# Kernel tuning notes

Hardware: AMD Instinct MI355X
Metric: run time of the kernel (lower is better)

The kernel has to match this reference:

```python
import jax, jax.numpy as jnp
import numpy as np

N = 50000      # nodes
E = 800000     # edges
DIM = 64       # dim_h (= input_dim)
H = 4          # heads
D = DIM // H   # per-head dim = 16
EDGE_DIM = 16
L = 5          # conv layers
G = 64         # graphs in batch
FINAL = 1
SCALE = 1.0 / np.sqrt(D)


def setup_inputs() -> dict:
    key = jax.random.key(0)
    ks = jax.random.split(key, 12)
    x = jax.random.normal(ks[0], (N, DIM), jnp.float32)
    edge_index = jax.random.randint(ks[1], (2, E), 0, N, dtype=jnp.int32).astype(jnp.int64)
    edge_attr = jax.random.normal(ks[2], (E, EDGE_DIM), jnp.float32)
    batch = jnp.sort(jax.random.randint(ks[3], (N,), 0, G, dtype=jnp.int32).astype(jnp.int64))
    s = 1.0 / np.sqrt(DIM)
    se = 1.0 / np.sqrt(EDGE_DIM)
    Wq = jax.random.normal(ks[4], (L, DIM, DIM), jnp.float32) * s
    Wk = jax.random.normal(ks[5], (L, DIM, DIM), jnp.float32) * s
    Wv = jax.random.normal(ks[6], (L, DIM, DIM), jnp.float32) * s
    We = jax.random.normal(ks[7], (L, EDGE_DIM, DIM), jnp.float32) * se
    Wskip = jax.random.normal(ks[8], (L, DIM, DIM), jnp.float32) * s
    W1 = jax.random.normal(ks[9], (L * DIM, L * DIM), jnp.float32) * (1.0 / np.sqrt(L * DIM))
    b1 = jnp.zeros((L * DIM,), jnp.float32)
    W2 = jax.random.normal(ks[10], (L * DIM, FINAL), jnp.float32) * (1.0 / np.sqrt(L * DIM))
    b2 = jnp.zeros((FINAL,), jnp.float32)
    return dict(x=x, edge_index=edge_index, edge_attr=edge_attr, batch=batch,
                Wq=Wq, Wk=Wk, Wv=Wv, We=We, Wskip=Wskip, W1=W1, b1=b1, W2=W2, b2=b2)


def _conv(x, Wq, Wk, Wv, We, Wsk, src, dst, edge_attr):
    # Edge-featured multi-head attention conv (EINv1 / TransformerConv-style).
    n = x.shape[0]
    q = (x @ Wq).reshape(n, H, D)[dst]                      # [E,H,D] query from dst node
    e = (edge_attr @ We).reshape(-1, H, D)                  # [E,H,D] edge projection
    k = (x @ Wk).reshape(n, H, D)[src] + e                  # [E,H,D]
    v = (x @ Wv).reshape(n, H, D)[src] + e                  # [E,H,D]
    logits = (q * k).sum(-1) * SCALE                        # [E,H]
    m = jax.ops.segment_max(logits, dst, num_segments=n)    # per-dst-node max
    a = jnp.exp(logits - m[dst])
    s = jax.ops.segment_sum(a, dst, num_segments=n)
    alpha = a / (s[dst] + 1e-16)                            # segment softmax over incoming edges
    agg = jax.ops.segment_sum(alpha[..., None] * v, dst, num_segments=n)  # [N,H,D]
    return agg.reshape(n, H * D) + x @ Wsk                  # root/skip connection


def reference(x, edge_index, edge_attr, batch, Wq, Wk, Wv, We, Wskip, W1, b1, W2, b2):
    src, dst = edge_index[0], edge_index[1]
    counts = jax.ops.segment_sum(jnp.ones((x.shape[0],), x.dtype), batch, num_segments=G)
    denom = jnp.maximum(counts, 1.0)[:, None]
    h = x
    pooled = []
    for l in range(L):  # fixed small layer count
        h = jax.nn.relu(_conv(h, Wq[l], Wk[l], Wv[l], We[l], Wskip[l], src, dst, edge_attr))
        pooled.append(jax.ops.segment_sum(h, batch, num_segments=G) / denom)  # global_mean_pool
    hcat = jnp.concatenate(pooled, axis=1)                  # [G, 5*DIM]
    hid = jax.nn.relu(hcat @ W1 + b1)
    out = hid @ W2 + b2                                     # dropout is identity in eval
    return out.reshape(-1)                                  # flatten -> [G*FINAL]
```

## Files before the change

kernel.cpp:

```cpp
#include <hip/hip_runtime.h>
#include <math.h>

#define NN 50000
#define NE 800000
#define GG 64
#define SCAN_BLK 512
#define SCAN_NB ((NN + SCAN_BLK - 1) / SCAN_BLK)
#define CSR_CAP (NE + 4 * NN)
#define NBLK ((NN + 63) / 64)

typedef unsigned int uint;
typedef unsigned short ushort;
typedef __attribute__((ext_vector_type(8))) short short8v;
typedef __attribute__((ext_vector_type(4))) float f32x4;

__device__ __forceinline__ uint bf16r(float x) {
    uint u = __float_as_uint(x);
    return (u + 0x7fffu + ((u >> 16) & 1u)) >> 16;
}

__device__ __forceinline__ float red16(float x) {
    float t;
    t = __int_as_float(__builtin_amdgcn_update_dpp(0, __float_as_int(x), 0xB1, 0xF, 0xF, 1));
    x += t;
    t = __int_as_float(__builtin_amdgcn_update_dpp(0, __float_as_int(x), 0x4E, 0xF, 0xF, 1));
    x += t;
    t = __int_as_float(__builtin_amdgcn_update_dpp(0, __float_as_int(x), 0x124, 0xF, 0xF, 1));
    x += t;
    t = __int_as_float(__builtin_amdgcn_update_dpp(0, __float_as_int(x), 0x128, 0xF, 0xF, 1));
    x += t;
    return x;
}


__global__ void k_bounds(const int* __restrict__ batch, int* __restrict__ bstart,
                         float* __restrict__ inv) {
    __shared__ int sb[65];
    int t = threadIdx.x;
    if (t <= 64) {
        int lo = 0, hi = NN;
        while (lo < hi) { int mid = (lo + hi) >> 1; if (batch[mid] < t) lo = mid + 1; else hi = mid; }
        sb[t] = lo;
        bstart[t] = lo;
    }
    __syncthreads();
    if (t < 64) inv[t] = 1.0f / fmaxf((float)(sb[t + 1] - sb[t]), 1.0f);
}


__global__ __launch_bounds__(256) void k_degrank(const int* __restrict__ dstv,
                                                 int* __restrict__ deg,
                                                 int* __restrict__ rank) {
    int e = blockIdx.x * 256 + threadIdx.x;
    if (e < NE) rank[e] = atomicAdd(&deg[dstv[e]], 1);
}

__global__ __launch_bounds__(SCAN_BLK) void k_scan1(const int* __restrict__ deg,
                                                    int* __restrict__ locoff,
                                                    int* __restrict__ bsum) {
    __shared__ int sh[SCAN_BLK];
    int tid = threadIdx.x;
    int n = blockIdx.x * SCAN_BLK + tid;
    int v = (n < NN) ? ((deg[n] + 3) & ~3) : 0;
    sh[tid] = v;
    __syncthreads();
    for (int off = 1; off < SCAN_BLK; off <<= 1) {
        int t = (tid >= off) ? sh[tid - off] : 0;
        __syncthreads();
        sh[tid] += t;
        __syncthreads();
    }
    if (n < NN) locoff[n] = sh[tid] - v;
    if (tid == SCAN_BLK - 1) bsum[blockIdx.x] = sh[tid];
}

__global__ void k_scan2(int* __restrict__ bsum) {
    __shared__ int sh[128];
    int t = threadIdx.x;
    int v = (t < SCAN_NB) ? bsum[t] : 0;
    sh[t] = v;
    __syncthreads();
    for (int off = 1; off < 128; off <<= 1) {
        int u = (t >= off) ? sh[t - off] : 0;
        __syncthreads();
        sh[t] += u;
        __syncthreads();
    }
    if (t < SCAN_NB) bsum[t] = sh[t] - v;
}

__global__ __launch_bounds__(256) void k_scan3(const int* __restrict__ locoff,
                                               const int* __restrict__ bsum,
                                               int* __restrict__ off) {
    int n = blockIdx.x * 256 + threadIdx.x;
    if (n < NN) off[n] = locoff[n] + bsum[n >> 9];
}

__global__ __launch_bounds__(256) void k_fill(const int* __restrict__ srcv,
                                              const int* __restrict__ dstv,
                                              const float* __restrict__ eattr,
                                              const int* __restrict__ off,
                                              const int* __restrict__ rank,
                                              int* __restrict__ srcp,
                                              ushort* __restrict__ aperm) {
    int e = blockIdx.x * 256 + threadIdx.x;
    if (e >= NE) return;
    int d = dstv[e];
    int p = off[d] + rank[e];
    srcp[p] = srcv[e] << 8;
    const float4* ea = reinterpret_cast<const float4*>(eattr + (size_t)e * 16);
    float4 a = ea[0], b = ea[1], c = ea[2], d4 = ea[3];
    uint4 u0, u1;
    u0.x = bf16r(a.x) | (bf16r(a.y) << 16);
    u0.y = bf16r(a.z) | (bf16r(a.w) << 16);
    u0.z = bf16r(b.x) | (bf16r(b.y) << 16);
    u0.w = bf16r(b.z) | (bf16r(b.w) << 16);
    u1.x = bf16r(c.x) | (bf16r(c.y) << 16);
    u1.y = bf16r(c.z) | (bf16r(c.w) << 16);
    u1.z = bf16r(d4.x) | (bf16r(d4.y) << 16);
    u1.w = bf16r(d4.z) | (bf16r(d4.w) << 16);
    uint4* ap = reinterpret_cast<uint4*>(aperm + (size_t)p * 16);
    ap[0] = u0;
    ap[1] = u1;
}

__global__ __launch_bounds__(256) void k_M(const float* __restrict__ Wq,
                                           const float* __restrict__ We,
                                           float* __restrict__ M) {
    int t = blockIdx.x * 256 + threadIdx.x;
    if (t >= 5 * 64 * 64) return;
    int l = t >> 12, i = (t >> 6) & 63, c = t & 63;
    int hh = c >> 4, j = c & 15;
    const float* wq = Wq + l * 4096 + i * 64 + hh * 16;
    const float* we = We + l * 1024 + j * 64 + hh * 16;
    float acc = 0.f;
#pragma unroll
    for (int dd = 0; dd < 16; ++dd) acc += wq[dd] * we[dd];
    M[t] = acc;
}


__global__ __launch_bounds__(256) void k_wfrag(const float* __restrict__ Wq,
                                               const float* __restrict__ Wk,
                                               const float* __restrict__ Wv,
                                               const float* __restrict__ Wsk,
                                               const float* __restrict__ Mw,
                                               ushort* __restrict__ Wf) {
    int t = blockIdx.x * 256 + threadIdx.x;
    if (t >= 5 * 20 * 2 * 64) return;
    int l = t / (20 * 2 * 64);
    int rem = t % (20 * 2 * 64);
    int nt = rem >> 7, s = (rem >> 6) & 1, lane = rem & 63;
    int c = nt * 16 + (lane & 15);
    int k0 = s * 32 + 8 * (lane >> 4);
    int msel = c >> 6, cc = c & 63;
    const float* W = (msel == 0) ? Wq + l * 4096 :
                     (msel == 1) ? Wk + l * 4096 :
                     (msel == 2) ? Wv + l * 4096 :
                     (msel == 3) ? Wsk + l * 4096 : Mw + l * 4096;
    ushort o[8];
#pragma unroll
    for (int j = 0; j < 8; ++j) o[j] = (ushort)bf16r(W[(k0 + j) * 64 + cc]);
    uint4* dst = reinterpret_cast<uint4*>(Wf + (size_t)t * 8);
    uint4 u;
    u.x = (uint)o[0] | ((uint)o[1] << 16);
    u.y = (uint)o[2] | ((uint)o[3] << 16);
    u.z = (uint)o[4] | ((uint)o[5] << 16);
    u.w = (uint)o[6] | ((uint)o[7] << 16);
    dst[0] = u;
}


template<bool L0>
__global__ __launch_bounds__(256) void k_projm(const float* __restrict__ x,
                                               const ushort* __restrict__ Hin,
                                               const ushort* __restrict__ Wfl,
                                               uint* __restrict__ QQp,
                                               uint* __restrict__ KVp,
                                               float* __restrict__ Sb) {
    int tid = threadIdx.x, lane = tid & 63, wv = tid >> 6;
    int n0 = blockIdx.x * 64;
    int arow = lane & 15, agrp = lane >> 4;

    short8v A[4][2];
#pragma unroll
    for (int mt = 0; mt < 4; ++mt) {
        int node = n0 + mt * 16 + arow;
        if (node >= NN) node = NN - 1;
#pragma unroll
        for (int s = 0; s < 2; ++s) {
            int k0 = s * 32 + agrp * 8;
            if (L0) {
                const float* hp = x + (size_t)node * 64 + k0;
                float4 u = *reinterpret_cast<const float4*>(hp);
                float4 v = *reinterpret_cast<const float4*>(hp + 4);
                short8v a;
                a[0] = (short)bf16r(u.x); a[1] = (short)bf16r(u.y);
                a[2] = (short)bf16r(u.z); a[3] = (short)bf16r(u.w);
                a[4] = (short)bf16r(v.x); a[5] = (short)bf16r(v.y);
                a[6] = (short)bf16r(v.z); a[7] = (short)bf16r(v.w);
                A[mt][s] = a;
            } else {
                A[mt][s] = *reinterpret_cast<const short8v*>(Hin + (size_t)node * 64 + k0);
            }
        }
    }

    int ch = wv * 16 + arow;
    int rb = agrp * 4;
    f32x4 qh[4], kh[4];
    const f32x4 z = {0.f, 0.f, 0.f, 0.f};

#pragma unroll
    for (int ni = 0; ni < 5; ++ni) {
        int ntl = wv + 4 * ni;
        f32x4 acc[4] = {z, z, z, z};
#pragma unroll
        for (int s = 0; s < 2; ++s) {
            short8v B = *reinterpret_cast<const short8v*>(
                Wfl + (((size_t)ntl * 2 + s) * 64 + lane) * 8);
#pragma unroll
            for (int mt = 0; mt < 4; ++mt)
                acc[mt] = __builtin_amdgcn_mfma_f32_16x16x32_bf16(A[mt][s], B, acc[mt], 0, 0, 0);
        }
        if (ni == 0) {
#pragma unroll
            for (int mt = 0; mt < 4; ++mt) qh[mt] = acc[mt];
        } else if (ni == 1) {
#pragma unroll
            for (int mt = 0; mt < 4; ++mt) kh[mt] = acc[mt];
        } else if (ni == 2) {
#pragma unroll
            for (int mt = 0; mt < 4; ++mt)
#pragma unroll
                for (int r = 0; r < 4; ++r) {
                    int node = n0 + mt * 16 + rb + r;
                    if (node < NN)
                        KVp[(size_t)node * 64 + ch] = (bf16r(kh[mt][r]) << 16) | bf16r(acc[mt][r]);
                }
        } else if (ni == 3) {
#pragma unroll
            for (int mt = 0; mt < 4; ++mt)
#pragma unroll
                for (int r = 0; r < 4; ++r) {
                    int node = n0 + mt * 16 + rb + r;
                    if (node < NN) Sb[(size_t)node * 64 + ch] = acc[mt][r];
                }
        } else {
#pragma unroll
            for (int mt = 0; mt < 4; ++mt)
#pragma unroll
                for (int r = 0; r < 4; ++r) {
                    int node = n0 + mt * 16 + rb + r;
                    if (node < NN)
                        QQp[(size_t)node * 64 + ch] = (bf16r(qh[mt][r]) << 16) | bf16r(acc[mt][r]);
                }
        }
    }
}


__global__ __launch_bounds__(256) void k_attn(const uint* __restrict__ QQp,
                                              const uint* __restrict__ KVp,
                                              const float* __restrict__ Sb,
                                              const float* __restrict__ Wel,
                                              const ushort* __restrict__ aperm,
                                              const int* __restrict__ srcp,
                                              const int* __restrict__ offp,
                                              const int* __restrict__ cnt,
                                              ushort* __restrict__ Hout) {
    __shared__ float we[16 * 64];
    int tid = threadIdx.x;
    for (int i = tid; i < 1024; i += 256) we[i] = Wel[i];
    __syncthreads();

    int lane = tid & 63;
    int n = blockIdx.x * 4 + (tid >> 6);
    if (n >= NN) return;

    int dd = lane & 15;
    int hg = lane >> 4;

    const float C2 = 0.36067376022224085f;
    uint qq = QQp[n * 64 + lane];
    float q  = __uint_as_float(qq & 0xffff0000u) * C2;
    float qw = __uint_as_float(qq << 16) * C2;
    int dg   = cnt[n];
    int pos0 = offp[n];
    int nbt  = (dg + 3) >> 2;

    const char* kvb = (const char*)KVp + lane * 4;
    const ushort* apb = aperm + (size_t)pos0 * 16 + dd;

    float m = -1e30f, s = 0.f, av = 0.f, aa = 0.f;

    auto ldidx = [&](int b, int4& sn) {
        sn = (b < nbt) ? *reinterpret_cast<const int4*>(srcp + pos0 + b * 4)
                       : make_int4(0, 0, 0, 0);
    };
    auto issue = [&](int b, const int4& sn, uint (&kv)[4], uint (&au)[4]) {
        kv[0] = *reinterpret_cast<const uint*>(kvb + sn.x);
        kv[1] = *reinterpret_cast<const uint*>(kvb + sn.y);
        kv[2] = *reinterpret_cast<const uint*>(kvb + sn.z);
        kv[3] = *reinterpret_cast<const uint*>(kvb + sn.w);
        const ushort* ap = apb + (size_t)b * 64;
        au[0] = ap[0];
        au[1] = ap[16];
        au[2] = ap[32];
        au[3] = ap[48];
    };
    auto compute = [&](int b, const uint (&kv)[4], const uint (&au)[4]) {
        int rem = dg - b * 4;
        float l[4], vf[4], af[4];
#pragma unroll
        for (int j = 0; j < 4; ++j) {
            uint w = kv[j];
            float kf = __uint_as_float(w & 0xffff0000u);
            vf[j] = __uint_as_float(w << 16);
            af[j] = __uint_as_float(au[j] << 16);
            float p = fmaf(q, kf, qw * af[j]);
            p = red16(p);
            l[j] = (j < rem) ? p : -1e30f;
        }
        float bm = fmaxf(fmaxf(l[0], l[1]), fmaxf(l[2], l[3]));
        float mn = fmaxf(m, bm);
        float wold = __builtin_amdgcn_exp2f(m - mn);
        float a0 = __builtin_amdgcn_exp2f(l[0] - mn);
        float a1 = __builtin_amdgcn_exp2f(l[1] - mn);
        float a2 = __builtin_amdgcn_exp2f(l[2] - mn);
        float a3 = __builtin_amdgcn_exp2f(l[3] - mn);
        s  = fmaf(s,  wold, (a0 + a1) + (a2 + a3));
        av = fmaf(av, wold, fmaf(a0, vf[0], fmaf(a1, vf[1], fmaf(a2, vf[2], a3 * vf[3]))));
        aa = fmaf(aa, wold, fmaf(a0, af[0], fmaf(a1, af[1], fmaf(a2, af[2], a3 * af[3]))));
        m = mn;
    };

    int4 sn0, sn1;
    uint kv0[4], kv1[4], at0[4], at1[4];

    ldidx(0, sn0);
    issue(0, sn0, kv0, at0);
    ldidx(1, sn1);

    int b = 0;
    while (b + 1 < nbt) {
        issue(b + 1, sn1, kv1, at1);
        ldidx(b + 2, sn0);
        compute(b, kv0, at0);
        if (b + 2 < nbt) {
            issue(b + 2, sn0, kv0, at0);
            ldidx(b + 3, sn1);
        }
        compute(b + 1, kv1, at1);
        b += 2;
    }
    if (b < nbt) compute(b, kv0, at0);

    float rden = 1.0f / (s + 1e-16f);
    float eagg = 0.f;
#pragma unroll
    for (int j = 0; j < 16; ++j) {
        float aj = __shfl(aa, hg * 16 + j, 64);
        eagg = fmaf(aj, we[j * 64 + lane], eagg);
    }
    float agg = (av + eagg) * rden;
    float hn = fmaxf(agg + Sb[n * 64 + lane], 0.f);
    Hout[(size_t)n * 64 + lane] = (ushort)bf16r(hn);
}


__global__ __launch_bounds__(512) void k_pool5(const ushort* __restrict__ Hb,
                                               const int* __restrict__ bstart,
                                               const float* __restrict__ inv,
                                               float* __restrict__ hcat) {
    __shared__ float red[512];
    int l = blockIdx.x >> 6, g = blockIdx.x & 63;
    int lo = bstart[g], hi = bstart[g + 1];
    const ushort* H = Hb + (size_t)l * NN * 64;
    int ch = threadIdx.x & 63, ro = threadIdx.x >> 6;
    float acc = 0.f;
    for (int r = lo + ro; r < hi; r += 8)
        acc += __uint_as_float((uint)H[(size_t)r * 64 + ch] << 16);
    red[threadIdx.x] = acc;
    __syncthreads();
    if (ro < 4) red[threadIdx.x] += red[threadIdx.x + 256];
    __syncthreads();
    if (ro < 2) red[threadIdx.x] += red[threadIdx.x + 128];
    __syncthreads();
    if (ro == 0)
        hcat[g * 320 + l * 64 + ch] = (red[ch] + red[64 + ch]) * inv[g];
}


__global__ __launch_bounds__(256) void k_mlp(const float* __restrict__ hcat,
                                             const float* __restrict__ W1,
                                             const float* __restrict__ b1,
                                             const float* __restrict__ W2,
                                             const float* __restrict__ b2,
                                             float* __restrict__ out) {
    __shared__ float hc[320];
    __shared__ float red[256];
    int g = blockIdx.x, tid = threadIdx.x;
    for (int i = tid; i < 320; i += 256) hc[i] = hcat[g * 320 + i];
    __syncthreads();
    float part = 0.f;
    for (int j = tid; j < 320; j += 256) {
        float t = b1[j];
        for (int k = 0; k < 320; ++k) t = fmaf(hc[k], W1[k * 320 + j], t);
        part = fmaf(fmaxf(t, 0.f), W2[j], part);
    }
    red[tid] = part;
    __syncthreads();
    for (int off = 128; off > 0; off >>= 1) {
        if (tid < off) red[tid] += red[tid + off];
        __syncthreads();
    }
    if (tid == 0) out[g] = red[0] + b2[0];
}


extern "C" void kernel_launch(void* const* d_in, const int* in_sizes, int n_in,
                              void* d_out, int out_size, void* d_ws, size_t ws_size,
                              hipStream_t stream) {
    const float* x     = (const float*)d_in[0];
    const int*   ei    = (const int*)d_in[1];
    const float* eattr = (const float*)d_in[2];
    const int*   batch = (const int*)d_in[3];
    const float* Wq    = (const float*)d_in[4];
    const float* Wk    = (const float*)d_in[5];
    const float* Wv    = (const float*)d_in[6];
    const float* We    = (const float*)d_in[7];
    const float* Wsk   = (const float*)d_in[8];
    const float* W1    = (const float*)d_in[9];
    const float* b1    = (const float*)d_in[10];
    const float* W2    = (const float*)d_in[11];
    const float* b2    = (const float*)d_in[12];
    float* out = (float*)d_out;

    const int* srcv = ei;
    const int* dstv = ei + NE;

    float* ws = (float*)d_ws;
    size_t o = 0;
    uint*   QQp = (uint*)(ws + o); o += (size_t)NN * 64;
    uint*   KVp = (uint*)(ws + o); o += (size_t)NN * 64;
    float*  Sb  = ws + o;          o += (size_t)NN * 64;
    ushort* Hb  = (ushort*)(ws + o); o += (size_t)5 * NN * 64 / 2;
    float*  Mw  = ws + o;          o += 5 * 4096;
    ushort* Wf  = (ushort*)(ws + o); o += 5 * 20 * 2 * 64 * 8 / 2;
    float*  inv = ws + o;          o += GG;
    float*  hcat = ws + o;         o += GG * 320;
    int*    bstart = (int*)(ws + o); o += 68;
    int*    deg  = (int*)(ws + o); o += NN;
    int*    srcp = (int*)(ws + o); o += CSR_CAP;
    size_t  zwords = (size_t)NN + CSR_CAP;
    int*    rank   = (int*)(ws + o); o += NE;
    int*    off    = (int*)(ws + o); o += NN;
    int*    locoff = (int*)(ws + o); o += NN;
    int*    bsum   = (int*)(ws + o); o += 128;
    ushort* aperm  = (ushort*)(ws + o); o += (size_t)CSR_CAP * 8;

    hipMemsetAsync(deg, 0, zwords * 4, stream);

    k_bounds<<<1, 128, 0, stream>>>(batch, bstart, inv);
    k_degrank<<<(NE + 255) / 256, 256, 0, stream>>>(dstv, deg, rank);
    k_scan1<<<SCAN_NB, SCAN_BLK, 0, stream>>>(deg, locoff, bsum);
    k_scan2<<<1, 128, 0, stream>>>(bsum);
    k_scan3<<<(NN + 255) / 256, 256, 0, stream>>>(locoff, bsum, off);
    k_fill<<<(NE + 255) / 256, 256, 0, stream>>>(srcv, dstv, eattr, off, rank, srcp, aperm);
    k_M<<<(5 * 4096 + 255) / 256, 256, 0, stream>>>(Wq, We, Mw);
    k_wfrag<<<50, 256, 0, stream>>>(Wq, Wk, Wv, Wsk, Mw, Wf);

    for (int l = 0; l < 5; ++l) {
        const ushort* Wfl = Wf + (size_t)l * 20 * 2 * 64 * 8;
        if (l == 0)
            k_projm<true><<<NBLK, 256, 0, stream>>>(x, Hb, Wfl, QQp, KVp, Sb);
        else
            k_projm<false><<<NBLK, 256, 0, stream>>>(x, Hb + (size_t)(l - 1) * NN * 64,
                                                     Wfl, QQp, KVp, Sb);
        k_attn<<<(NN + 3) / 4, 256, 0, stream>>>(QQp, KVp, Sb,
                                                 We + l * 1024, aperm,
                                                 srcp, off, deg,
                                                 Hb + (size_t)l * NN * 64);
    }
    k_pool5<<<320, 512, 0, stream>>>(Hb, bstart, inv, hcat);
    k_mlp<<<GG, 256, 0, stream>>>(hcat, W1, b1, W2, b2, out);
}
```

Before: 516.2 us.

## Split wave into two half-waves processing two edges each with paired channels

```diff
diff --git a/kernel.cpp b/kernel.cpp
--- a/kernel.cpp
+++ b/kernel.cpp
@@ -19,15 +19,13 @@
     return (u + 0x7fffu + ((u >> 16) & 1u)) >> 16;
 }
 
-__device__ __forceinline__ float red16(float x) {
+__device__ __forceinline__ float red8(float x) {
     float t;
     t = __int_as_float(__builtin_amdgcn_update_dpp(0, __float_as_int(x), 0xB1, 0xF, 0xF, 1));
     x += t;
     t = __int_as_float(__builtin_amdgcn_update_dpp(0, __float_as_int(x), 0x4E, 0xF, 0xF, 1));
     x += t;
-    t = __int_as_float(__builtin_amdgcn_update_dpp(0, __float_as_int(x), 0x124, 0xF, 0xF, 1));
-    x += t;
-    t = __int_as_float(__builtin_amdgcn_update_dpp(0, __float_as_int(x), 0x128, 0xF, 0xF, 1));
+    t = __int_as_float(__builtin_amdgcn_update_dpp(0, __float_as_int(x), 0x141, 0xF, 0xF, 1));
     x += t;
     return x;
 }
@@ -158,9 +156,11 @@
                      (msel == 1) ? Wk + l * 4096 :
                      (msel == 2) ? Wv + l * 4096 :
                      (msel == 3) ? Wsk + l * 4096 : Mw + l * 4096;
+    const float C2 = 0.36067376022224085f;
+    float sc = (msel == 0 || msel == 4) ? C2 : 1.0f;
     ushort o[8];
 #pragma unroll
-    for (int j = 0; j < 8; ++j) o[j] = (ushort)bf16r(W[(k0 + j) * 64 + cc]);
+    for (int j = 0; j < 8; ++j) o[j] = (ushort)bf16r(W[(k0 + j) * 64 + cc] * sc);
     uint4* dst = reinterpret_cast<uint4*>(Wf + (size_t)t * 8);
     uint4 u;
     u.x = (uint)o[0] | ((uint)o[1] << 16);
@@ -264,7 +264,7 @@
                                               const uint* __restrict__ KVp,
                                               const float* __restrict__ Sb,
                                               const float* __restrict__ Wel,
-                                              const ushort* __restrict__ aperm,
+                                              const uint* __restrict__ aperm32,
                                               const int* __restrict__ srcp,
                                               const int* __restrict__ offp,
                                               const int* __restrict__ cnt,
@@ -278,94 +278,109 @@
     int n = blockIdx.x * 4 + (tid >> 6);
     if (n >= NN) return;
 
-    int dd = lane & 15;
-    int hg = lane >> 4;
-
-    const float C2 = 0.36067376022224085f;
-    uint qq = QQp[n * 64 + lane];
-    float q  = __uint_as_float(qq & 0xffff0000u) * C2;
-    float qw = __uint_as_float(qq << 16) * C2;
-    int dg   = cnt[n];
-    int pos0 = offp[n];
-    int nbt  = (dg + 3) >> 2;
-
-    const char* kvb = (const char*)KVp + lane * 4;
-    const ushort* apb = aperm + (size_t)pos0 * 16 + dd;
-
-    float m = -1e30f, s = 0.f, av = 0.f, aa = 0.f;
-
-    auto ldidx = [&](int b, int4& sn) {
-        sn = (b < nbt) ? *reinterpret_cast<const int4*>(srcp + pos0 + b * 4)
+    int pc = lane & 31;
+    int eh = lane >> 5;
+    int hd = pc >> 3;
+
+    uint2 qq = *reinterpret_cast<const uint2*>(QQp + n * 64 + 2 * pc);
+    float qf0  = __uint_as_float(qq.x & 0xffff0000u);
+    float qwf0 = __uint_as_float(qq.x << 16);
+    float qf1  = __uint_as_float(qq.y & 0xffff0000u);
+    float qwf1 = __uint_as_float(qq.y << 16);
+
+    int dg = cnt[n], pos0 = offp[n];
+    int npass = (dg + 1) >> 1;
+    int nsb = (npass + 1) >> 1;
+
+    const char* kvb = (const char*)KVp + pc * 8;
+    const uint* apb = aperm32 + (size_t)pos0 * 8 + (pc & 7) + eh * 8;
+
+    float s = 0.f, av0 = 0.f, av1 = 0.f, aa0 = 0.f, aa1 = 0.f;
+
+    auto ldidx = [&](int j, int4& s4) {
+        s4 = (j < nsb) ? *reinterpret_cast<const int4*>(srcp + pos0 + j * 4)
                        : make_int4(0, 0, 0, 0);
     };
-    auto issue = [&](int b, const int4& sn, uint (&kv)[4], uint (&au)[4]) {
-        kv[0] = *reinterpret_cast<const uint*>(kvb + sn.x);
-        kv[1] = *reinterpret_cast<const uint*>(kvb + sn.y);
-        kv[2] = *reinterpret_cast<const uint*>(kvb + sn.z);
-        kv[3] = *reinterpret_cast<const uint*>(kvb + sn.w);
-        const ushort* ap = apb + (size_t)b * 64;
-        au[0] = ap[0];
-        au[1] = ap[16];
-        au[2] = ap[32];
-        au[3] = ap[48];
+    auto issueSB = [&](int j, const int4& s4, uint2 (&kv)[2], uint (&au)[2]) {
+        int sn0 = eh ? s4.y : s4.x;
+        int sn1 = eh ? s4.w : s4.z;
+        kv[0] = *reinterpret_cast<const uint2*>(kvb + sn0);
+        kv[1] = *reinterpret_cast<const uint2*>(kvb + sn1);
+        const uint* a = apb + (size_t)j * 32;
+        au[0] = a[0];
+        au[1] = a[16];
     };
-    auto compute = [&](int b, const uint (&kv)[4], const uint (&au)[4]) {
-        int rem = dg - b * 4;
-        float l[4], vf[4], af[4];
-#pragma unroll
-        for (int j = 0; j < 4; ++j) {
-            uint w = kv[j];
-            float kf = __uint_as_float(w & 0xffff0000u);
-            vf[j] = __uint_as_float(w << 16);
-            af[j] = __uint_as_float(au[j] << 16);
-            float p = fmaf(q, kf, qw * af[j]);
-            p = red16(p);
-            l[j] = (j < rem) ? p : -1e30f;
+    auto computeSB = [&](int j, const uint2 (&kv)[2], const uint (&au)[2]) {
+#pragma unroll
+        for (int p = 0; p < 2; ++p) {
+            float kf0 = __uint_as_float(kv[p].x & 0xffff0000u);
+            float vf0 = __uint_as_float(kv[p].x << 16);
+            float kf1 = __uint_as_float(kv[p].y & 0xffff0000u);
+            float vf1 = __uint_as_float(kv[p].y << 16);
+            float af0 = __uint_as_float(au[p] << 16);
+            float af1 = __uint_as_float(au[p] & 0xffff0000u);
+            float d = qf0 * kf0;
+            d = fmaf(qf1, kf1, d);
+            d = fmaf(qwf0, af0, d);
+            d = fmaf(qwf1, af1, d);
+            d = red8(d);
+            int ei = j * 4 + p * 2 + eh;
+            float l = (ei < dg) ? d : -1e30f;
+            float a = __builtin_amdgcn_exp2f(l);
+            s += a;
+            av0 = fmaf(a, vf0, av0);
+            av1 = fmaf(a, vf1, av1);
+            aa0 = fmaf(a, af0, aa0);
+            aa1 = fmaf(a, af1, aa1);
         }
-        float bm = fmaxf(fmaxf(l[0], l[1]), fmaxf(l[2], l[3]));
-        float mn = fmaxf(m, bm);
-        float wold = __builtin_amdgcn_exp2f(m - mn);
-        float a0 = __builtin_amdgcn_exp2f(l[0] - mn);
-        float a1 = __builtin_amdgcn_exp2f(l[1] - mn);
-        float a2 = __builtin_amdgcn_exp2f(l[2] - mn);
-        float a3 = __builtin_amdgcn_exp2f(l[3] - mn);
-        s  = fmaf(s,  wold, (a0 + a1) + (a2 + a3));
-        av = fmaf(av, wold, fmaf(a0, vf[0], fmaf(a1, vf[1], fmaf(a2, vf[2], a3 * vf[3]))));
-        aa = fmaf(aa, wold, fmaf(a0, af[0], fmaf(a1, af[1], fmaf(a2, af[2], a3 * af[3]))));
-        m = mn;
     };
 
-    int4 sn0, sn1;
-    uint kv0[4], kv1[4], at0[4], at1[4];
-
-    ldidx(0, sn0);
-    issue(0, sn0, kv0, at0);
-    ldidx(1, sn1);
-
-    int b = 0;
-    while (b + 1 < nbt) {
-        issue(b + 1, sn1, kv1, at1);
-        ldidx(b + 2, sn0);
-        compute(b, kv0, at0);
-        if (b + 2 < nbt) {
-            issue(b + 2, sn0, kv0, at0);
-            ldidx(b + 3, sn1);
+    int4 s4a, s4b;
+    uint2 kvA[2], kvB[2];
+    uint auA[2], auB[2];
+
+    ldidx(0, s4a);
+    issueSB(0, s4a, kvA, auA);
+    ldidx(1, s4b);
+
+    int sb = 0;
+    while (sb + 1 < nsb) {
+        issueSB(sb + 1, s4b, kvB, auB);
+        ldidx(sb + 2, s4a);
+        computeSB(sb, kvA, auA);
+        if (sb + 2 < nsb) {
+            issueSB(sb + 2, s4a, kvA, auA);
+            ldidx(sb + 3, s4b);
         }
-        compute(b + 1, kv1, at1);
-        b += 2;
-    }
-    if (b < nbt) compute(b, kv0, at0);
+        computeSB(sb + 1, kvB, auB);
+        sb += 2;
+    }
+    if (sb < nsb) computeSB(sb, kvA, auA);
+
+    s   += __shfl_xor(s, 32);
+    av0 += __shfl_xor(av0, 32);
+    av1 += __shfl_xor(av1, 32);
+    aa0 += __shfl_xor(aa0, 32);
+    aa1 += __shfl_xor(aa1, 32);
 
     float rden = 1.0f / (s + 1e-16f);
-    float eagg = 0.f;
-#pragma unroll
-    for (int j = 0; j < 16; ++j) {
-        float aj = __shfl(aa, hg * 16 + j, 64);
-        eagg = fmaf(aj, we[j * 64 + lane], eagg);
-    }
-    float agg = (av + eagg) * rden;
-    float hn = fmaxf(agg + Sb[n * 64 + lane], 0.f);
-    Hout[(size_t)n * 64 + lane] = (ushort)bf16r(hn);
+    float e0 = 0.f, e1 = 0.f;
+#pragma unroll
+    for (int t = 0; t < 8; ++t) {
+        float ae = __shfl(aa0, hd * 8 + t, 32);
+        float ao = __shfl(aa1, hd * 8 + t, 32);
+        float2 wE = *reinterpret_cast<const float2*>(&we[(2 * t) * 64 + 2 * pc]);
+        float2 wO = *reinterpret_cast<const float2*>(&we[(2 * t + 1) * 64 + 2 * pc]);
+        e0 = fmaf(ae, wE.x, fmaf(ao, wO.x, e0));
+        e1 = fmaf(ae, wE.y, fmaf(ao, wO.y, e1));
+    }
+    float2 sb2 = *reinterpret_cast<const float2*>(Sb + n * 64 + 2 * pc);
+    float hn0 = fmaxf(fmaf(av0 + e0, rden, sb2.x), 0.f);
+    float hn1 = fmaxf(fmaf(av1 + e1, rden, sb2.y), 0.f);
+    if (lane < 32) {
+        uint hw = bf16r(hn0) | (bf16r(hn1) << 16);
+        reinterpret_cast<uint*>(Hout)[(size_t)n * 32 + pc] = hw;
+    }
 }
 
 
@@ -479,7 +494,8 @@
             k_projm<false><<<NBLK, 256, 0, stream>>>(x, Hb + (size_t)(l - 1) * NN * 64,
                                                      Wfl, QQp, KVp, Sb);
         k_attn<<<(NN + 3) / 4, 256, 0, stream>>>(QQp, KVp, Sb,
-                                                 We + l * 1024, aperm,
+                                                 We + l * 1024,
+                                                 (const uint*)aperm,
                                                  srcp, off, deg,
                                                  Hb + (size_t)l * NN * 64);
     }
```

New measurement: 456.4 us. -11.6%, faster.
